# Kernel tuning notes

Measured on AMD Instinct MI355X. Metric: run time of the kernel, lower is better.

## Reference

```python
import jax, jax.numpy as jnp
import numpy as np

LRELU_ALPHA = 0.2   # LeakyReLU negative slope (alpha init arg)
NEG_INF = -9e15     # masking constant used by standard GAT layers

B, N, NFEAT, NHID, NHEAD, NPRED = 16, 1024, 16, 32, 4, 12


def setup_inputs() -> dict:
    key = jax.random.key(0)
    ks = jax.random.split(key, 8)
    x = jax.random.normal(ks[0], (B, N, NFEAT), dtype=jnp.float32)
    adj = jax.random.randint(ks[1], (N, N), 0, 2, dtype=jnp.int32)
    s = 0.1
    W = jax.random.normal(ks[2], (NHEAD, NFEAT, NHID), dtype=jnp.float32) * s
    a_src = jax.random.normal(ks[3], (NHEAD, NHID), dtype=jnp.float32) * s
    a_dst = jax.random.normal(ks[4], (NHEAD, NHID), dtype=jnp.float32) * s
    W_out = jax.random.normal(ks[5], (NHEAD * NHID, NPRED), dtype=jnp.float32) * s
    a_out_src = jax.random.normal(ks[6], (NPRED,), dtype=jnp.float32) * s
    a_out_dst = jax.random.normal(ks[7], (NPRED,), dtype=jnp.float32) * s
    return {"x": x, "adj": adj, "W": W, "a_src": a_src, "a_dst": a_dst,
            "W_out": W_out, "a_out_src": a_out_src, "a_out_dst": a_out_dst}


def reference(x, adj, W, a_src, a_dst, W_out, a_out_src, a_out_dst):
    # Eval mode: all F.dropout calls are identity.
    mask = adj > 0  # [N, N], broadcast over batch (and heads)

    # --- multi-head GAT layer (concat=True), all heads vectorized ---
    Wh = jnp.einsum('bnf,hfk->bhnk', x, W)                 # [B,H,N,K]
    f_src = jnp.einsum('bhnk,hk->bhn', Wh, a_src)          # [B,H,N]
    f_dst = jnp.einsum('bhnk,hk->bhn', Wh, a_dst)
    e = jax.nn.leaky_relu(f_src[..., :, None] + f_dst[..., None, :], LRELU_ALPHA)
    attn = jax.nn.softmax(jnp.where(mask, e, NEG_INF), axis=-1)  # [B,H,N,N]
    h = jax.nn.elu(jnp.einsum('bhnm,bhmk->bhnk', attn, Wh))      # concat=True -> ELU
    b, H, n, k = h.shape
    h = jnp.transpose(h, (0, 2, 1, 3)).reshape(b, n, H * k)  # concat heads, dim=2

    # --- output GAT layer (concat=False) ---
    Wh2 = h @ W_out                                        # [B,N,npred]
    g_src = Wh2 @ a_out_src                                # [B,N]
    g_dst = Wh2 @ a_out_dst
    e2 = jax.nn.leaky_relu(g_src[:, :, None] + g_dst[:, None, :], LRELU_ALPHA)
    attn2 = jax.nn.softmax(jnp.where(mask, e2, NEG_INF), axis=-1)
    out = jax.nn.elu(jnp.einsum('bnm,bmp->bnp', attn2, Wh2))  # outer F.elu in STGAT
    return out.reshape(b, -1)                              # [B, N*npred]
```

## Files before the change

kernel.cpp:

```cpp
#include <hip/hip_runtime.h>
#include <cmath>

#define B_    16
#define N_    1024
#define NHID_ 32
#define NHEAD_ 4
#define NPRED_ 12
#define ALPHA 0.2f
#define LOG2E 1.442695041f

typedef __attribute__((ext_vector_type(8)))  short    short8;
typedef __attribute__((ext_vector_type(4)))  float    floatx4;
typedef __attribute__((ext_vector_type(2)))  float    float2v;
typedef __attribute__((ext_vector_type(4)))  unsigned uintx4;

__device__ __forceinline__ float bs2f(unsigned short s) {
    return __uint_as_float(((unsigned)s) << 16);
}
__device__ __forceinline__ short f2bs(float f) {
    unsigned u = __float_as_uint(f);
    unsigned r = (u + 0x7fffu + ((u >> 16) & 1u)) >> 16;
    return (short)r;
}
__device__ __forceinline__ float ldin(const void* p, long i, int isbf) {
    if (isbf) return bs2f(((const unsigned short*)p)[i]);
    return ((const float*)p)[i];
}
__device__ __forceinline__ float fexp2(float x) {
#if __has_builtin(__builtin_amdgcn_exp2f)
    return __builtin_amdgcn_exp2f(x);
#else
    return __expf(x * 0.6931471805599453f);
#endif
}
__device__ __forceinline__ unsigned pk2(unsigned u0, unsigned u1) {
#if __has_builtin(__builtin_amdgcn_perm)
    return __builtin_amdgcn_perm(u1, u0, 0x07060302u);
#else
    return (u0 >> 16) | (u1 & 0xffff0000u);
#endif
}
__device__ __forceinline__ float2v vmax2(float2v a, float2v b) {
#if __has_builtin(__builtin_elementwise_max)
    return __builtin_elementwise_max(a, b);
#else
    float2v r; r.x = fmaxf(a.x, b.x); r.y = fmaxf(a.y, b.y); return r;
#endif
}
__device__ __forceinline__ float2v vfma2(float2v a, float2v b, float2v c) {
#if __has_builtin(__builtin_elementwise_fma)
    return __builtin_elementwise_fma(a, b, c);
#else
    float2v r; r.x = __builtin_fmaf(a.x, b.x, c.x); r.y = __builtin_fmaf(a.y, b.y, c.y); return r;
#endif
}
__device__ __forceinline__ int detect_isbf(const unsigned short* xu) {
    int lane = threadIdx.x & 63;
    uint4 v = ((const uint4*)xu)[lane];
    unsigned wv[4] = {v.x, v.y, v.z, v.w};
    bool any = false;
#pragma unroll
    for (int i = 0; i < 4; ++i) {
        any |= (((wv[i] & 0xffffu) >> 7) & 0xffu) >= 160u;
        any |= (((wv[i] >> 16) >> 7) & 0xffu) >= 160u;
    }
    return __popcll(__ballot(any)) < 8;
}

__global__ __launch_bounds__(256) void k01_prep_wh(
    const unsigned short* __restrict__ xu, const int* __restrict__ adj,
    const void* __restrict__ x, const void* __restrict__ W,
    const void* __restrict__ a_src, const void* __restrict__ a_dst,
    unsigned short* __restrict__ bias,
    short* __restrict__ WhB, float* __restrict__ f_src, float* __restrict__ f_dst)
{
    int tid = threadIdx.x;
    if (blockIdx.x < 512) {
        int gid = blockIdx.x * 256 + tid;
        long base = (long)gid * 8;
        int4 a0 = *(const int4*)(adj + base);
        int4 a1 = *(const int4*)(adj + base + 4);
        uint4 wv;
        wv.x = (a0.x ? 0u : 0xFF80u) | (a0.y ? 0u : 0xFF800000u);
        wv.y = (a0.z ? 0u : 0xFF80u) | (a0.w ? 0u : 0xFF800000u);
        wv.z = (a1.x ? 0u : 0xFF80u) | (a1.y ? 0u : 0xFF800000u);
        wv.w = (a1.z ? 0u : 0xFF80u) | (a1.w ? 0u : 0xFF800000u);
        *(uint4*)(bias + base) = wv;
        return;
    }
    int isbf = detect_isbf(xu);
    __shared__ float Ws[16][32];
    __shared__ float xs[32][17];
    __shared__ float as_s[32], ad_s[32];
    __shared__ float Wa_s[16], Wad_s[16];
    int bid = blockIdx.x - 512;
    int bh = bid >> 5;
    int n0 = (bid & 31) * 32;
    int b  = bh >> 2, hh = bh & 3;

    for (int idx = tid; idx < 512; idx += 256)
        Ws[idx >> 5][idx & 31] = ldin(W, hh * 512 + idx, isbf);
    if (tid < 32) {
        as_s[tid] = ldin(a_src, hh * 32 + tid, isbf);
        ad_s[tid] = ldin(a_dst, hh * 32 + tid, isbf);
    }
    for (int idx = tid; idx < 512; idx += 256) {
        int r = idx >> 4, f = idx & 15;
        xs[r][f] = ldin(x, ((long)(b * N_ + n0 + r)) * 16 + f, isbf);
    }
    __syncthreads();

    if (tid < 32) {
        int f = tid & 15;
        const float* av = (tid < 16) ? as_s : ad_s;
        float s = 0.f;
#pragma unroll
        for (int kk = 0; kk < 32; ++kk) s += Ws[f][kk] * av[kk];
        ((tid < 16) ? Wa_s : Wad_s)[f] = s;
    }
    __syncthreads();

    if (tid < 32) {
        float fs = 0.f, fd = 0.f;
#pragma unroll
        for (int f = 0; f < 16; ++f) {
            fs += xs[tid][f] * Wa_s[f];
            fd += xs[tid][f] * Wad_s[f];
        }
        int n = n0 + tid;
        f_src[bh * N_ + n] = fs * LOG2E;
        f_dst[bh * N_ + n] = fd * LOG2E;
    }

    int k = tid & 31, rb = tid >> 5;
#pragma unroll
    for (int it = 0; it < 4; ++it) {
        int r = it * 8 + rb;
        float acc = 0.f;
#pragma unroll
        for (int f = 0; f < 16; ++f) acc += xs[r][f] * Ws[f][k];
        int n = n0 + r;
        int kstep = n >> 5, quad = (n >> 3) & 3, jj = n & 7;
        int t = k >> 4, l = quad * 16 + (k & 15);
        WhB[((((size_t)bh * 32 + kstep) * 2 + t) * 64 + l) * 8 + jj] = f2bs(acc);
    }
}

__global__ __launch_bounds__(256) void k2_attn1(
    const float* __restrict__ f_src, const float* __restrict__ f_dst,
    const unsigned short* __restrict__ bias, const short* __restrict__ WhB,
    float* __restrict__ h_cat)
{
    __shared__ float fdst_s[N_];
    __shared__ float wmax[4];
    __shared__ float Sh[2][2][16];
    __shared__ float xch[2][64][8];
    int bid = blockIdx.x;
    int bh = bid >> 5;
    int tile = bid & 31;
    int tid = threadIdx.x;
    int w = tid >> 6, lane = tid & 63;
    int rh = w & 1, ch = w >> 1;

    float lmax = -INFINITY;
    for (int idx = tid; idx < N_; idx += 256) {
        float v = f_dst[bh * N_ + idx];
        fdst_s[idx] = v;
        lmax = fmaxf(lmax, v);
    }
#pragma unroll
    for (int m = 32; m; m >>= 1) lmax = fmaxf(lmax, __shfl_xor(lmax, m, 64));
    if (lane == 0) wmax[w] = lmax;
    __syncthreads();
    float maxfd = fmaxf(fmaxf(wmax[0], wmax[1]), fmaxf(wmax[2], wmax[3]));

    int i0 = tile * 32 + rh * 16;
    int r = lane & 15, q = lane >> 4;

    float fsr = f_src[bh * N_ + i0 + r];
    float Mv = fsr + maxfd;
    float M = fmaxf(Mv, ALPHA * Mv);
    float2v a1v; a1v.x = fsr - M;          a1v.y = a1v.x;
    float2v a2v; a2v.x = ALPHA * fsr - M;  a2v.y = a2v.x;
    float2v alv; alv.x = ALPHA;            alv.y = ALPHA;
    float2v s2 = {};

    floatx4 acc0 = {}, acc1 = {};
    const unsigned short* brow = bias + (size_t)(i0 + r) * N_ + ch * 512 + q * 8;
    const float* fdp = fdst_s + ch * 512 + q * 8;

    uint4  bu_n = *(const uint4*)(brow);
    float4 fa_n = *(const float4*)(fdp);
    float4 fb_n = *(const float4*)(fdp + 4);

#pragma unroll 4
    for (int kk = 0; kk < 16; ++kk) {
        uint4 bu = bu_n; float4 fda = fa_n; float4 fdb = fb_n;
        if (kk < 15) {
            bu_n = *(const uint4*)(brow + (kk + 1) * 32);
            fa_n = *(const float4*)(fdp + (kk + 1) * 32);
            fb_n = *(const float4*)(fdp + (kk + 1) * 32 + 4);
        }
        unsigned bw[4] = {bu.x, bu.y, bu.z, bu.w};
        float fdx[8] = {fda.x, fda.y, fda.z, fda.w, fdb.x, fdb.y, fdb.z, fdb.w};
        unsigned dpk[4];
#pragma unroll
        for (int p = 0; p < 4; ++p) {
            float2v fd2; fd2.x = fdx[2 * p]; fd2.y = fdx[2 * p + 1];
            float2v b2;  b2.x = __uint_as_float(bw[p] << 16);
                         b2.y = __uint_as_float(bw[p] & 0xffff0000u);
            float2v t1 = a1v + fd2;
            float2v t2 = vfma2(alv, fd2, a2v);
            float2v arg = vmax2(t1, t2) + b2;
            float2v pv; pv.x = fexp2(arg.x); pv.y = fexp2(arg.y);
            s2 += pv;
            dpk[p] = pk2(__float_as_uint(pv.x) + 0x8000u,
                         __float_as_uint(pv.y) + 0x8000u);
        }
        uintx4 du; du[0] = dpk[0]; du[1] = dpk[1]; du[2] = dpk[2]; du[3] = dpk[3];
        short8 afr = __builtin_bit_cast(short8, du);
        const short* bbase = WhB + ((((size_t)bh * 32 + ch * 16 + kk) * 2) * 64 + lane) * 8;
        short8 bfr0 = *(const short8*)(bbase);
        short8 bfr1 = *(const short8*)(bbase + 512);
        acc0 = __builtin_amdgcn_mfma_f32_16x16x32_bf16(afr, bfr0, acc0, 0, 0, 0);
        acc1 = __builtin_amdgcn_mfma_f32_16x16x32_bf16(afr, bfr1, acc1, 0, 0, 0);
    }

    float s = s2.x + s2.y;
    s += __shfl_xor(s, 16, 64);
    s += __shfl_xor(s, 32, 64);
    if (lane < 16) Sh[rh][ch][lane] = s;
    if (ch == 1) {
#pragma unroll
        for (int i = 0; i < 4; ++i) {
            xch[rh][lane][i]     = acc0[i];
            xch[rh][lane][4 + i] = acc1[i];
        }
    }
    __syncthreads();
    if (ch == 0) {
#pragma unroll
        for (int i = 0; i < 4; ++i) {
            acc0[i] += xch[rh][lane][i];
            acc1[i] += xch[rh][lane][4 + i];
        }
        int bb = bh >> 2, head = bh & 3;
#pragma unroll
        for (int reg = 0; reg < 4; ++reg) {
            int row = q * 4 + reg;
            float rsv = 1.f / (Sh[rh][0][row] + Sh[rh][1][row]);
            float* hrow = &h_cat[((size_t)(bb * N_ + i0 + row)) * 128 + head * 32];
            float v0 = acc0[reg] * rsv;
            hrow[r]      = v0 > 0.f ? v0 : expm1f(v0);
            float v1 = acc1[reg] * rsv;
            hrow[16 + r] = v1 > 0.f ? v1 : expm1f(v1);
        }
    }
}

__global__ __launch_bounds__(256) void k3_out_proj(
    const unsigned short* __restrict__ xu,
    const float* __restrict__ h_cat, const void* __restrict__ W_out,
    const void* __restrict__ a_out_src, const void* __restrict__ a_out_dst,
    short* __restrict__ Wh2B, float* __restrict__ g_src, float* __restrict__ g_dst)
{
    int isbf = detect_isbf(xu);
    __shared__ float WoT[16][132];
    __shared__ float hs[16][132];
    __shared__ float aos[16], aod[16];
    int bid = blockIdx.x;
    int b = bid >> 6;
    int n0 = (bid & 63) * 16;
    int tid = threadIdx.x;

    for (int idx = tid; idx < 2048; idx += 256) {
        int p = idx >> 7, c = idx & 127;
        WoT[p][c] = (p < NPRED_) ? ldin(W_out, c * NPRED_ + p, isbf) : 0.f;
    }
    if (tid < 16) {
        aos[tid] = (tid < NPRED_) ? ldin(a_out_src, tid, isbf) : 0.f;
        aod[tid] = (tid < NPRED_) ? ldin(a_out_dst, tid, isbf) : 0.f;
    }
    for (int idx = tid; idx < 512; idx += 256) {
        int rr = idx >> 5, c4 = (idx & 31) * 4;
        *(float4*)&hs[rr][c4] = *(const float4*)&h_cat[((size_t)(b * N_ + n0 + rr)) * 128 + c4];
    }
    __syncthreads();

    int r = tid >> 4, p = tid & 15;
    float acc = 0.f;
#pragma unroll 8
    for (int c4 = 0; c4 < 128; c4 += 4) {
        float4 hv = *(const float4*)&hs[r][c4];
        float4 wv = *(const float4*)&WoT[p][c4];
        acc += hv.x * wv.x + hv.y * wv.y + hv.z * wv.z + hv.w * wv.w;
    }

    float t1 = acc * aos[p], t2 = acc * aod[p];
#pragma unroll
    for (int m = 8; m; m >>= 1) {
        t1 += __shfl_xor(t1, m, 64);
        t2 += __shfl_xor(t2, m, 64);
    }
    int n = n0 + r;
    if (p == 0) {
        g_src[b * N_ + n] = t1 * LOG2E;
        g_dst[b * N_ + n] = t2 * LOG2E;
    }
    int kstep = n >> 5, quad = (n >> 3) & 3, jj = n & 7;
    short val = (p == 15) ? (short)0x3F80 : f2bs(acc);
    Wh2B[(((size_t)b * 32 + kstep) * 64 + quad * 16 + p) * 8 + jj] = val;
}

__global__ __launch_bounds__(256) void k4_attn2(
    const unsigned short* __restrict__ xu,
    const float* __restrict__ g_src, const float* __restrict__ g_dst,
    const unsigned short* __restrict__ bias, const short* __restrict__ Wh2B,
    void* __restrict__ out)
{
    int isbf = detect_isbf(xu);
    __shared__ float gdst_s[N_];
    __shared__ float wmax[4];
    __shared__ float xch[3][64][4];
    int bid = blockIdx.x;
    int b = bid >> 6;
    int tile = bid & 63;
    int tid = threadIdx.x;
    int ch = tid >> 6, lane = tid & 63;

    float lmax = -INFINITY;
    for (int idx = tid; idx < N_; idx += 256) {
        float v = g_dst[b * N_ + idx];
        gdst_s[idx] = v;
        lmax = fmaxf(lmax, v);
    }
#pragma unroll
    for (int m = 32; m; m >>= 1) lmax = fmaxf(lmax, __shfl_xor(lmax, m, 64));
    if (lane == 0) wmax[ch] = lmax;
    __syncthreads();
    float maxgd = fmaxf(fmaxf(wmax[0], wmax[1]), fmaxf(wmax[2], wmax[3]));

    int i0 = tile * 16;
    int r = lane & 15, q = lane >> 4;

    float gsr = g_src[b * N_ + i0 + r];
    float Mv = gsr + maxgd;
    float M = fmaxf(Mv, ALPHA * Mv);
    float2v a1v; a1v.x = gsr - M;          a1v.y = a1v.x;
    float2v a2v; a2v.x = ALPHA * gsr - M;  a2v.y = a2v.x;
    float2v alv; alv.x = ALPHA;            alv.y = ALPHA;

    floatx4 acc = {};
    const unsigned short* brow = bias + (size_t)(i0 + r) * N_ + ch * 256 + q * 8;
    const float* fdp = gdst_s + ch * 256 + q * 8;

    uint4  bu_n = *(const uint4*)(brow);
    float4 fa_n = *(const float4*)(fdp);
    float4 fb_n = *(const float4*)(fdp + 4);

#pragma unroll 4
    for (int kk = 0; kk < 8; ++kk) {
        uint4 bu = bu_n; float4 fda = fa_n; float4 fdb = fb_n;
        if (kk < 7) {
            bu_n = *(const uint4*)(brow + (kk + 1) * 32);
            fa_n = *(const float4*)(fdp + (kk + 1) * 32);
            fb_n = *(const float4*)(fdp + (kk + 1) * 32 + 4);
        }
        unsigned bw[4] = {bu.x, bu.y, bu.z, bu.w};
        float fdx[8] = {fda.x, fda.y, fda.z, fda.w, fdb.x, fdb.y, fdb.z, fdb.w};
        unsigned dpk[4];
#pragma unroll
        for (int p = 0; p < 4; ++p) {
            float2v fd2; fd2.x = fdx[2 * p]; fd2.y = fdx[2 * p + 1];
            float2v b2;  b2.x = __uint_as_float(bw[p] << 16);
                         b2.y = __uint_as_float(bw[p] & 0xffff0000u);
            float2v t1 = a1v + fd2;
            float2v t2 = vfma2(alv, fd2, a2v);
            float2v arg = vmax2(t1, t2) + b2;
            float2v pv; pv.x = fexp2(arg.x); pv.y = fexp2(arg.y);
            dpk[p] = pk2(__float_as_uint(pv.x) + 0x8000u,
                         __float_as_uint(pv.y) + 0x8000u);
        }
        uintx4 du; du[0] = dpk[0]; du[1] = dpk[1]; du[2] = dpk[2]; du[3] = dpk[3];
        short8 afr = __builtin_bit_cast(short8, du);
        short8 bfr = *(const short8*)(Wh2B + (((size_t)b * 32 + ch * 8 + kk) * 64 + lane) * 8);
        acc = __builtin_amdgcn_mfma_f32_16x16x32_bf16(afr, bfr, acc, 0, 0, 0);
    }

    if (ch != 0) {
#pragma unroll
        for (int i = 0; i < 4; ++i) xch[ch - 1][lane][i] = acc[i];
    }
    __syncthreads();
    if (ch == 0) {
#pragma unroll
        for (int t = 0; t < 3; ++t)
#pragma unroll
            for (int i = 0; i < 4; ++i) acc[i] += xch[t][lane][i];
        int srclane = (lane & 48) + 15;
#pragma unroll
        for (int reg = 0; reg < 4; ++reg) {
            int row = q * 4 + reg;
            float Srow = __shfl(acc[reg], srclane, 64);
            float v = acc[reg] / Srow;
            float o = v > 0.f ? v : expm1f(v);
            if (r < NPRED_) {
                size_t idx = (size_t)b * (N_ * NPRED_) + (size_t)(i0 + row) * NPRED_ + r;
                if (isbf) ((unsigned short*)out)[idx] = (unsigned short)f2bs(o);
                else      ((float*)out)[idx] = o;
            }
        }
    }
}

extern "C" void kernel_launch(void* const* d_in, const int* in_sizes, int n_in,
                              void* d_out, int out_size, void* d_ws, size_t ws_size,
                              hipStream_t stream)
{
    (void)in_sizes; (void)n_in; (void)out_size; (void)ws_size;
    const void* x      = d_in[0];
    const int*  adj    = (const int*)d_in[1];
    const void* W      = d_in[2];
    const void* a_src  = d_in[3];
    const void* a_dst  = d_in[4];
    const void* W_out  = d_in[5];
    const void* a_osrc = d_in[6];
    const void* a_odst = d_in[7];
    const unsigned short* xu = (const unsigned short*)x;

    char* ws = (char*)d_ws;
    short* WhB   = (short*)(ws);
    float* f_src = (float*)(ws + (4 << 20));
    float* f_dst = (float*)(ws + (4 << 20) + (256 << 10));
    float* h_cat = (float*)(ws + (4 << 20) + (512 << 10));
    short* Wh2B  = (short*)(ws + (12 << 20) + (512 << 10));
    float* g_src = (float*)(ws + (13 << 20));
    float* g_dst = (float*)(ws + (13 << 20) + (64 << 10));
    unsigned short* bias = (unsigned short*)(ws + (14 << 20));

    hipLaunchKernelGGL(k01_prep_wh, dim3(2560), dim3(256), 0, stream,
                       xu, adj, x, W, a_src, a_dst, bias, WhB, f_src, f_dst);
    hipLaunchKernelGGL(k2_attn1,    dim3(2048), dim3(256), 0, stream,
                       f_src, f_dst, bias, WhB, h_cat);
    hipLaunchKernelGGL(k3_out_proj, dim3(1024), dim3(256), 0, stream,
                       xu, h_cat, W_out, a_osrc, a_odst, Wh2B, g_src, g_dst);
    hipLaunchKernelGGL(k4_attn2,    dim3(1024), dim3(256), 0, stream,
                       xu, g_src, g_dst, bias, Wh2B, d_out);
}
```

Baseline: 127.2 us.

## Store concat hidden as bf16, vectorize input loads, reorder block indices

The concatenated first-layer output is now stored as bf16 instead of fp32, which halves the intermediate's write and read traffic between the attention and output-projection kernels. Loads of W, x and W_out are vectorized into shared memory. Block-index decomposition in both attention kernels is swapped so consecutive blocks cover different batch/heads, which changes how the shared bias matrix is reused in cache. The bf16 rounding of the hidden activations adds a small precision loss.

```diff
diff --git a/kernel.cpp b/kernel.cpp
--- a/kernel.cpp
+++ b/kernel.cpp
@@ -9,10 +9,12 @@
 #define ALPHA 0.2f
 #define LOG2E 1.442695041f
 
-typedef __attribute__((ext_vector_type(8)))  short    short8;
-typedef __attribute__((ext_vector_type(4)))  float    floatx4;
-typedef __attribute__((ext_vector_type(2)))  float    float2v;
-typedef __attribute__((ext_vector_type(4)))  unsigned uintx4;
+typedef __attribute__((ext_vector_type(8)))  short          short8;
+typedef __attribute__((ext_vector_type(4)))  float          floatx4;
+typedef __attribute__((ext_vector_type(2)))  float          float2v;
+typedef __attribute__((ext_vector_type(4)))  unsigned       uintx4;
+typedef __attribute__((ext_vector_type(4)))  unsigned short ushort4v;
+typedef __attribute__((ext_vector_type(8)))  unsigned short ushort8v;
 
 __device__ __forceinline__ float bs2f(unsigned short s) {
     return __uint_as_float(((unsigned)s) << 16);
@@ -98,15 +100,38 @@
     int n0 = (bid & 31) * 32;
     int b  = bh >> 2, hh = bh & 3;
 
-    for (int idx = tid; idx < 512; idx += 256)
-        Ws[idx >> 5][idx & 31] = ldin(W, hh * 512 + idx, isbf);
+    if (!isbf) {
+        const float* Wf = (const float*)W + hh * 512;
+        if (tid < 128) {
+            float4 v = *(const float4*)(Wf + tid * 4);
+            int f = (tid * 4) >> 5, k = (tid * 4) & 31;
+            Ws[f][k] = v.x; Ws[f][k+1] = v.y; Ws[f][k+2] = v.z; Ws[f][k+3] = v.w;
+        }
+        const float* xf = (const float*)x + ((long)(b * N_ + n0)) * 16;
+        if (tid < 128) {
+            float4 v = *(const float4*)(xf + tid * 4);
+            int r = tid >> 2, f = (tid & 3) * 4;
+            xs[r][f] = v.x; xs[r][f+1] = v.y; xs[r][f+2] = v.z; xs[r][f+3] = v.w;
+        }
+    } else {
+        const unsigned short* Wb = (const unsigned short*)W + hh * 512;
+        if (tid < 128) {
+            ushort4v v = *(const ushort4v*)(Wb + tid * 4);
+            int f = (tid * 4) >> 5, k = (tid * 4) & 31;
+            Ws[f][k] = bs2f(v[0]); Ws[f][k+1] = bs2f(v[1]);
+            Ws[f][k+2] = bs2f(v[2]); Ws[f][k+3] = bs2f(v[3]);
+        }
+        const unsigned short* xb = (const unsigned short*)x + ((long)(b * N_ + n0)) * 16;
+        if (tid < 64) {
+            ushort8v v = *(const ushort8v*)(xb + tid * 8);
+            int r = tid >> 1, f = (tid & 1) * 8;
+#pragma unroll
+            for (int i = 0; i < 8; ++i) xs[r][f + i] = bs2f(v[i]);
+        }
+    }
     if (tid < 32) {
         as_s[tid] = ldin(a_src, hh * 32 + tid, isbf);
         ad_s[tid] = ldin(a_dst, hh * 32 + tid, isbf);
-    }
-    for (int idx = tid; idx < 512; idx += 256) {
-        int r = idx >> 4, f = idx & 15;
-        xs[r][f] = ldin(x, ((long)(b * N_ + n0 + r)) * 16 + f, isbf);
     }
     __syncthreads();
 
@@ -149,15 +174,15 @@
 __global__ __launch_bounds__(256) void k2_attn1(
     const float* __restrict__ f_src, const float* __restrict__ f_dst,
     const unsigned short* __restrict__ bias, const short* __restrict__ WhB,
-    float* __restrict__ h_cat)
+    unsigned short* __restrict__ h2)
 {
     __shared__ float fdst_s[N_];
     __shared__ float wmax[4];
     __shared__ float Sh[2][2][16];
     __shared__ float xch[2][64][8];
     int bid = blockIdx.x;
-    int bh = bid >> 5;
-    int tile = bid & 31;
+    int bh = bid & 63;
+    int tile = bid >> 6;
     int tid = threadIdx.x;
     int w = tid >> 6, lane = tid & 63;
     int rh = w & 1, ch = w >> 1;
@@ -249,18 +274,20 @@
         for (int reg = 0; reg < 4; ++reg) {
             int row = q * 4 + reg;
             float rsv = 1.f / (Sh[rh][0][row] + Sh[rh][1][row]);
-            float* hrow = &h_cat[((size_t)(bb * N_ + i0 + row)) * 128 + head * 32];
+            unsigned short* hrow = &h2[((size_t)(bb * N_ + i0 + row)) * 128 + head * 32];
             float v0 = acc0[reg] * rsv;
-            hrow[r]      = v0 > 0.f ? v0 : expm1f(v0);
+            v0 = v0 > 0.f ? v0 : expm1f(v0);
+            hrow[r]      = (unsigned short)f2bs(v0);
             float v1 = acc1[reg] * rsv;
-            hrow[16 + r] = v1 > 0.f ? v1 : expm1f(v1);
+            v1 = v1 > 0.f ? v1 : expm1f(v1);
+            hrow[16 + r] = (unsigned short)f2bs(v1);
         }
     }
 }
 
 __global__ __launch_bounds__(256) void k3_out_proj(
     const unsigned short* __restrict__ xu,
-    const float* __restrict__ h_cat, const void* __restrict__ W_out,
+    const unsigned short* __restrict__ h2, const void* __restrict__ W_out,
     const void* __restrict__ a_out_src, const void* __restrict__ a_out_dst,
     short* __restrict__ Wh2B, float* __restrict__ g_src, float* __restrict__ g_dst)
 {
@@ -273,17 +300,41 @@
     int n0 = (bid & 63) * 16;
     int tid = threadIdx.x;
 
-    for (int idx = tid; idx < 2048; idx += 256) {
-        int p = idx >> 7, c = idx & 127;
-        WoT[p][c] = (p < NPRED_) ? ldin(W_out, c * NPRED_ + p, isbf) : 0.f;
+    if (!isbf) {
+        const float* Wf = (const float*)W_out;
+        for (int idx = tid; idx < 384; idx += 256) {
+            float4 v = *(const float4*)(Wf + idx * 4);
+            float vv[4] = {v.x, v.y, v.z, v.w};
+#pragma unroll
+            for (int i = 0; i < 4; ++i) {
+                int e = idx * 4 + i;
+                WoT[e % NPRED_][e / NPRED_] = vv[i];
+            }
+        }
+    } else {
+        const unsigned short* Wb = (const unsigned short*)W_out;
+        for (int idx = tid; idx < 192; idx += 256) {
+            ushort8v v = *(const ushort8v*)(Wb + idx * 8);
+#pragma unroll
+            for (int i = 0; i < 8; ++i) {
+                int e = idx * 8 + i;
+                WoT[e % NPRED_][e / NPRED_] = bs2f(v[i]);
+            }
+        }
+    }
+    if (tid < 128) {
+#pragma unroll
+        for (int p = NPRED_; p < 16; ++p) WoT[p][tid] = 0.f;
     }
     if (tid < 16) {
         aos[tid] = (tid < NPRED_) ? ldin(a_out_src, tid, isbf) : 0.f;
         aod[tid] = (tid < NPRED_) ? ldin(a_out_dst, tid, isbf) : 0.f;
     }
-    for (int idx = tid; idx < 512; idx += 256) {
-        int rr = idx >> 5, c4 = (idx & 31) * 4;
-        *(float4*)&hs[rr][c4] = *(const float4*)&h_cat[((size_t)(b * N_ + n0 + rr)) * 128 + c4];
+    {
+        ushort8v v = *(const ushort8v*)(h2 + ((size_t)(b * N_ + n0 + (tid >> 4))) * 128 + (tid & 15) * 8);
+        int r = tid >> 4, c8 = (tid & 15) * 8;
+#pragma unroll
+        for (int i = 0; i < 8; ++i) hs[r][c8 + i] = bs2f(v[i]);
     }
     __syncthreads();
 
@@ -323,8 +374,8 @@
     __shared__ float wmax[4];
     __shared__ float xch[3][64][4];
     int bid = blockIdx.x;
-    int b = bid >> 6;
-    int tile = bid & 63;
+    int b = bid & 15;
+    int tile = bid >> 4;
     int tid = threadIdx.x;
     int ch = tid >> 6, lane = tid & 63;
 
@@ -432,7 +483,7 @@
     short* WhB   = (short*)(ws);
     float* f_src = (float*)(ws + (4 << 20));
     float* f_dst = (float*)(ws + (4 << 20) + (256 << 10));
-    float* h_cat = (float*)(ws + (4 << 20) + (512 << 10));
+    unsigned short* h2 = (unsigned short*)(ws + (4 << 20) + (512 << 10));
     short* Wh2B  = (short*)(ws + (12 << 20) + (512 << 10));
     float* g_src = (float*)(ws + (13 << 20));
     float* g_dst = (float*)(ws + (13 << 20) + (64 << 10));
@@ -441,9 +492,9 @@
     hipLaunchKernelGGL(k01_prep_wh, dim3(2560), dim3(256), 0, stream,
                        xu, adj, x, W, a_src, a_dst, bias, WhB, f_src, f_dst);
     hipLaunchKernelGGL(k2_attn1,    dim3(2048), dim3(256), 0, stream,
-                       f_src, f_dst, bias, WhB, h_cat);
+                       f_src, f_dst, bias, WhB, h2);
     hipLaunchKernelGGL(k3_out_proj, dim3(1024), dim3(256), 0, stream,
-                       xu, h_cat, W_out, a_osrc, a_odst, Wh2B, g_src, g_dst);
+                       xu, h2, W_out, a_osrc, a_odst, Wh2B, g_src, g_dst);
     hipLaunchKernelGGL(k4_attn2,    dim3(1024), dim3(256), 0, stream,
                        xu, g_src, g_dst, bias, Wh2B, d_out);
 }
```

New measurement: 120.8 us. 1.05x faster.
